# Kernel tuning notes

Hardware: AMD Instinct MI355X
Metric: run time of the kernel (lower is better)

Reference implementation:

```python
import jax, jax.numpy as jnp
import numpy as np

N_NODES = 50000
N_EDGES = 800000
HIDDEN = 128
N_LAYERS = 3
N_MASKED = 25000
N_GRAPHS = 64


def setup_inputs() -> dict:
    key = jax.random.key(0)
    ks = jax.random.split(key, 8)
    scale = 1.0 / np.sqrt(HIDDEN)
    return {
        "x": jax.random.normal(ks[0], (N_NODES, HIDDEN), dtype=jnp.float32),
        "edge_index": jax.random.randint(ks[1], (2, N_EDGES), 0, N_NODES, dtype=jnp.int64),
        "mask": jax.random.randint(ks[2], (N_MASKED,), 0, N_NODES, dtype=jnp.int64),
        "batch": jnp.sort(jax.random.randint(ks[3], (N_MASKED,), 0, N_GRAPHS, dtype=jnp.int64)),
        "conv_w": jax.random.normal(ks[4], (N_LAYERS, HIDDEN, HIDDEN), dtype=jnp.float32) * scale,
        "conv_b": jnp.zeros((N_LAYERS, HIDDEN), dtype=jnp.float32),
        "lt1_w": jax.random.normal(ks[5], (HIDDEN,), dtype=jnp.float32) * scale,
        "lt1_b": jnp.zeros((1,), dtype=jnp.float32),
    }


def reference(x, edge_index, mask, batch, conv_w, conv_b, lt1_w, lt1_b):
    n = x.shape[0]
    # GCNConv: add self-loops, symmetric normalization D^-1/2 (A+I) D^-1/2
    loops = jnp.arange(n, dtype=edge_index.dtype)
    src = jnp.concatenate([edge_index[0], loops])
    dst = jnp.concatenate([edge_index[1], loops])
    deg = jax.ops.segment_sum(jnp.ones_like(src, dtype=x.dtype), dst, num_segments=n)
    dinv = jax.lax.rsqrt(deg)  # deg >= 1 because of self-loops
    norm = (dinv[src] * dinv[dst])[:, None]  # [E+N, 1]

    h = x
    for l in range(N_LAYERS):
        hw = h @ conv_w[l]                                  # [N, H]
        agg = jax.ops.segment_sum(hw[src] * norm, dst, num_segments=n)
        h = jax.nn.elu(agg + conv_b[l])                     # dropout is identity in eval mode

    xm = h[mask]                                            # [M, H] masked-node features
    pooled = jax.ops.segment_max(xm, batch, num_segments=N_GRAPHS)  # global_max_pool
    return pooled @ lt1_w[:, None] + lt1_b                  # [G, 1]
```

## Files before the change

### kernel.cpp

```cpp
#include <hip/hip_runtime.h>
#include <math.h>

#define N_NODES  50000
#define N_EDGES  800000
#define HIDDEN   128
#define N_LAYERS 3
#define N_MASKED 25000
#define N_GRAPHS 64

typedef __attribute__((ext_vector_type(8))) short bf16x8;
typedef __attribute__((ext_vector_type(4))) float f32x4;

__device__ __forceinline__ unsigned fmap(float f) {
    unsigned u = __float_as_uint(f);
    return (u & 0x80000000u) ? ~u : (u | 0x80000000u);
}
__device__ __forceinline__ float funmap(unsigned u) {
    return __uint_as_float((u & 0x80000000u) ? (u & 0x7FFFFFFFu) : ~u);
}

__device__ __forceinline__ unsigned pack_split(float x) {
    unsigned u = __float_as_uint(x);
    unsigned hi = (u + 0x7fffu + ((u >> 16) & 1u)) >> 16;
    float rem = x - __uint_as_float(hi << 16);
    unsigned v = __float_as_uint(rem);
    unsigned lo = (v + 0x7fffu + ((v >> 16) & 1u)) >> 16;
    return hi | (lo << 16);
}

__global__ void count_deg_kernel(const int* __restrict__ dst, unsigned* __restrict__ deg) {
    int i = blockIdx.x * blockDim.x + threadIdx.x;
    if (i < N_EDGES) atomicAdd(&deg[dst[i]], 1u);
}

__global__ void dinv_kernel(const unsigned* __restrict__ deg, float* __restrict__ dinv) {
    int i = blockIdx.x * blockDim.x + threadIdx.x;
    if (i < N_NODES) dinv[i] = rsqrtf((float)(deg[i] + 1u));
}

__global__ void scan_block_kernel(const unsigned* __restrict__ deg, unsigned* __restrict__ incl,
                                  unsigned* __restrict__ bsum) {
    __shared__ unsigned s[1024];
    int i = blockIdx.x * 1024 + threadIdx.x;
    unsigned v = (i < N_NODES) ? deg[i] : 0u;
    s[threadIdx.x] = v;
    __syncthreads();
    for (int off = 1; off < 1024; off <<= 1) {
        unsigned t = (threadIdx.x >= off) ? s[threadIdx.x - off] : 0u;
        __syncthreads();
        s[threadIdx.x] += t;
        __syncthreads();
    }
    if (i < N_NODES) incl[i] = s[threadIdx.x];
    if (threadIdx.x == 1023) bsum[blockIdx.x] = s[1023];
}

__global__ void scan_bsum_kernel(unsigned* __restrict__ bsum, int n) {
    if (blockIdx.x == 0 && threadIdx.x == 0) {
        unsigned run = 0;
        for (int i = 0; i < n; ++i) { unsigned t = bsum[i]; bsum[i] = run; run += t; }
    }
}

__global__ void scan_finalize_kernel(const unsigned* __restrict__ incl,
                                     const unsigned* __restrict__ bsum_ex,
                                     unsigned* __restrict__ row_ptr,
                                     unsigned* __restrict__ cursor) {
    int i = blockIdx.x * blockDim.x + threadIdx.x;
    if (i <= N_NODES) {
        unsigned v = (i == 0) ? 0u : incl[i - 1] + bsum_ex[(i - 1) >> 10];
        row_ptr[i] = v;
        if (i < N_NODES) cursor[i] = v;
    }
}

__global__ void fill_csr_kernel(const int* __restrict__ src, const int* __restrict__ dst,
                                unsigned* __restrict__ cursor, int* __restrict__ csr_src) {
    int e = blockIdx.x * blockDim.x + threadIdx.x;
    if (e < N_EDGES) {
        unsigned p = atomicAdd(&cursor[dst[e]], 1u);
        csr_src[p] = src[e];
    }
}

__global__ void wprep_kernel(const float* __restrict__ W,
                             unsigned short* __restrict__ Whi,
                             unsigned short* __restrict__ Wlo) {
    int idx = blockIdx.x * 256 + threadIdx.x;
    if (idx >= 3 * 16384) return;
    int j     = idx & 7;
    int lane  = (idx >> 3) & 63;
    int ct    = (idx >> 9) & 7;
    int ks    = (idx >> 12) & 3;
    int layer = idx >> 14;
    int k = ks * 32 + (lane >> 4) * 8 + j;
    int n = ct * 16 + (lane & 15);
    unsigned p = pack_split(W[layer * 16384 + k * 128 + n]);
    Whi[idx] = (unsigned short)(p & 0xffffu);
    Wlo[idx] = (unsigned short)(p >> 16);
}

__global__ void xpack_kernel(const float* __restrict__ x, unsigned* __restrict__ xp, int n) {
    int i = blockIdx.x * 256 + threadIdx.x;
    if (i < n) xp[i] = pack_split(x[i]);
}

template<int MODE>
__global__ __launch_bounds__(256) void mfma_gemm_kernel(const unsigned* __restrict__ Ap,
                                                        const unsigned short* __restrict__ Wh,
                                                        const unsigned short* __restrict__ Wl,
                                                        const float* __restrict__ dinv,
                                                        const float* __restrict__ bias,
                                                        const int* __restrict__ batch,
                                                        unsigned* __restrict__ gmax,
                                                        float* __restrict__ Out,
                                                        int nrows) {
    const int lane = threadIdx.x & 63;
    const int wv = threadIdx.x >> 6;
    const int rowBase = blockIdx.x * 64 + wv * 16;
    if (rowBase >= nrows) return;

    int arow = rowBase + (lane & 15);
    if (arow > nrows - 1) arow = nrows - 1;
    const unsigned* aptr = Ap + (size_t)arow * 128 + (lane >> 4) * 8;

    f32x4 acc[8];
    #pragma unroll
    for (int c = 0; c < 8; ++c) acc[c] = (f32x4){0.f, 0.f, 0.f, 0.f};

    #pragma unroll
    for (int ks = 0; ks < 4; ++ks) {
        uint4 pa0 = *(const uint4*)(aptr + ks * 32);
        uint4 pa1 = *(const uint4*)(aptr + ks * 32 + 4);
        unsigned pv[8] = {pa0.x, pa0.y, pa0.z, pa0.w, pa1.x, pa1.y, pa1.z, pa1.w};
        bf16x8 ah, al;
        #pragma unroll
        for (int j = 0; j < 8; ++j) {
            ah[j] = (short)(pv[j] & 0xffffu);
            al[j] = (short)(pv[j] >> 16);
        }
        const unsigned short* wbh = Wh + ks * 4096 + lane * 8;
        const unsigned short* wbl = Wl + ks * 4096 + lane * 8;
        #pragma unroll
        for (int ct = 0; ct < 8; ++ct) {
            bf16x8 bh = *(const bf16x8*)(wbh + ct * 512);
            bf16x8 bl = *(const bf16x8*)(wbl + ct * 512);
            acc[ct] = __builtin_amdgcn_mfma_f32_16x16x32_bf16(ah, bh, acc[ct], 0, 0, 0);
            acc[ct] = __builtin_amdgcn_mfma_f32_16x16x32_bf16(al, bh, acc[ct], 0, 0, 0);
            acc[ct] = __builtin_amdgcn_mfma_f32_16x16x32_bf16(ah, bl, acc[ct], 0, 0, 0);
        }
    }

    const int colBase = lane & 15;
    const int rgrp = lane >> 4;
    #pragma unroll
    for (int r = 0; r < 4; ++r) {
        int row = rowBase + rgrp * 4 + r;
        if (row >= nrows) continue;
        float d = 0.f;
        int bofs = 0;
        if (MODE == 0 || MODE == 1) d = dinv[row];
        if (MODE == 2) bofs = batch[row] * 128;
        #pragma unroll
        for (int ct = 0; ct < 8; ++ct) {
            int col = ct * 16 + colBase;
            float o = acc[ct][r];
            if (MODE == 0) {
                Out[(size_t)row * 128 + col] = o * d;
            } else {
                o += bias[col];
                o = o > 0.f ? o : expm1f(o);
                if (MODE == 1) Out[(size_t)row * 128 + col] = o * d;
                else           atomicMax(&gmax[bofs + col], fmap(o));
            }
        }
    }
}

template<int GMODE>
__global__ __launch_bounds__(256) void gather_kernel(const float* __restrict__ tab,
                                                     const unsigned* __restrict__ row_ptr,
                                                     const int* __restrict__ csr_src,
                                                     const float* __restrict__ dinv,
                                                     const float* __restrict__ bias,
                                                     float* __restrict__ outf,
                                                     unsigned* __restrict__ outp,
                                                     const int* __restrict__ nodes,
                                                     int n_items) {
    int wid = (blockIdx.x * blockDim.x + threadIdx.x) >> 6;
    int w = wid >> 1;
    if (w >= n_items) return;
    const int f = ((wid & 1) << 6) | (threadIdx.x & 63);
    const int v = nodes ? nodes[w] : w;

    const unsigned s0 = row_ptr[v], e0 = row_ptr[v + 1];
    const float* __restrict__ base = tab + f;

    float acc[8];
    #pragma unroll
    for (int j = 0; j < 8; ++j) acc[j] = 0.f;
    acc[0] = base[(size_t)v << 7];

    unsigned i = s0;
    if (i + 8 <= e0) {
        int idx[8];
        #pragma unroll
        for (int j = 0; j < 8; ++j) idx[j] = csr_src[i + j];
        for (; i + 16 <= e0; i += 8) {
            int nxt[8];
            #pragma unroll
            for (int j = 0; j < 8; ++j) nxt[j] = csr_src[i + 8 + j];
            #pragma unroll
            for (int j = 0; j < 8; ++j) acc[j] += base[(size_t)idx[j] << 7];
            #pragma unroll
            for (int j = 0; j < 8; ++j) idx[j] = nxt[j];
        }
        #pragma unroll
        for (int j = 0; j < 8; ++j) acc[j] += base[(size_t)idx[j] << 7];
        i += 8;
    }
    if (i + 4 <= e0) {
        #pragma unroll
        for (int j = 0; j < 4; ++j) acc[j] += base[(size_t)csr_src[i + j] << 7];
        i += 4;
    }
    for (; i < e0; ++i) acc[0] += base[(size_t)csr_src[i] << 7];

    float dv = dinv[v];
    float sumall = ((acc[0] + acc[1]) + (acc[2] + acc[3])) +
                   ((acc[4] + acc[5]) + (acc[6] + acc[7]));
    if (GMODE == 0) {
        float o = dv * sumall + bias[f];
        o = o > 0.f ? o : expm1f(o);
        outf[((size_t)w << 7) + f] = o * dv;
    } else {
        outp[((size_t)w << 7) + f] = pack_split(dv * sumall);
    }
}

__global__ void gmax_init_kernel(unsigned* __restrict__ gmax) {
    int i = blockIdx.x * blockDim.x + threadIdx.x;
    if (i < N_GRAPHS * 128) gmax[i] = 0x007FFFFFu;
}

__global__ void pool_finish_kernel(const unsigned* __restrict__ gmax,
                                   const float* __restrict__ w, const float* __restrict__ b,
                                   float* __restrict__ out) {
    const int g = blockIdx.x;
    const int f = threadIdx.x;
    float val = funmap(gmax[g * 128 + f]) * w[f];
    #pragma unroll
    for (int off = 32; off > 0; off >>= 1) val += __shfl_down(val, off);
    __shared__ float ps[2];
    if ((threadIdx.x & 63) == 0) ps[threadIdx.x >> 6] = val;
    __syncthreads();
    if (threadIdx.x == 0) out[g] = ps[0] + ps[1] + b[0];
}

extern "C" void kernel_launch(void* const* d_in, const int* in_sizes, int n_in,
                              void* d_out, int out_size, void* d_ws, size_t ws_size,
                              hipStream_t stream) {
    const float* x      = (const float*)d_in[0];
    const int*   ei     = (const int*)d_in[1];
    const int*   mask   = (const int*)d_in[2];
    const int*   batch  = (const int*)d_in[3];
    const float* conv_w = (const float*)d_in[4];
    const float* conv_b = (const float*)d_in[5];
    const float* lt1_w  = (const float*)d_in[6];
    const float* lt1_b  = (const float*)d_in[7];
    float* out = (float*)d_out;

    const int* e_src = ei;
    const int* e_dst = ei + N_EDGES;

    char* ws = (char*)d_ws;
    auto carve = [&](size_t bytes) { char* p = ws; ws += (bytes + 255) & ~(size_t)255; return p; };
    unsigned* deg     = (unsigned*)carve(N_NODES * 4);
    float*    dinv    = (float*)   carve(N_NODES * 4);
    unsigned* row_ptr = (unsigned*)carve((N_NODES + 1) * 4);
    unsigned* cursor  = (unsigned*)carve(N_NODES * 4);
    unsigned* bsum    = (unsigned*)carve(64 * 4);
    unsigned* gmax    = (unsigned*)carve(N_GRAPHS * 128 * 4);
    unsigned short* wph = (unsigned short*)carve(3 * 16384 * 2);
    unsigned short* wpl = (unsigned short*)carve(3 * 16384 * 2);
    int*      csr_src = (int*)     carve((size_t)N_EDGES * 4);
    char*     reg1    = carve((size_t)N_NODES * HIDDEN * 4);
    char*     reg2    = carve((size_t)N_NODES * HIDDEN * 4);
    unsigned* incl    = (unsigned*)csr_src;

    unsigned* xp    = (unsigned*)reg1;
    float*    bufB  = (float*)reg1;
    float*    bufB2 = (float*)reg1;
    float*    bufA  = (float*)reg2;
    unsigned* bufAp = (unsigned*)reg2;
    unsigned* bufCp = (unsigned*)reg2;

    const int NB_SCAN = (N_NODES + 1023) / 1024;

    hipMemsetAsync(deg, 0, N_NODES * sizeof(unsigned), stream);
    count_deg_kernel<<<(N_EDGES + 255) / 256, 256, 0, stream>>>(e_dst, deg);
    dinv_kernel<<<(N_NODES + 255) / 256, 256, 0, stream>>>(deg, dinv);
    scan_block_kernel<<<NB_SCAN, 1024, 0, stream>>>(deg, incl, bsum);
    scan_bsum_kernel<<<1, 64, 0, stream>>>(bsum, NB_SCAN);
    scan_finalize_kernel<<<(N_NODES + 256) / 256, 256, 0, stream>>>(incl, bsum, row_ptr, cursor);
    fill_csr_kernel<<<(N_EDGES + 255) / 256, 256, 0, stream>>>(e_src, e_dst, cursor, csr_src);
    gmax_init_kernel<<<(N_GRAPHS * 128 + 255) / 256, 256, 0, stream>>>(gmax);
    wprep_kernel<<<(3 * 16384 + 255) / 256, 256, 0, stream>>>(conv_w, wph, wpl);
    xpack_kernel<<<(N_NODES * HIDDEN + 255) / 256, 256, 0, stream>>>(x, xp, N_NODES * HIDDEN);

    const int GEMM_FULL = (N_NODES + 63) / 64;
    const int GEMM_MASK = (N_MASKED + 63) / 64;
    const int GA_FULL = (N_NODES * 2 * 64 + 255) / 256;
    const int GA_MASK = (N_MASKED * 2 * 64 + 255) / 256;

    mfma_gemm_kernel<0><<<GEMM_FULL, 256, 0, stream>>>(xp, wph, wpl, dinv, nullptr,
                                                       nullptr, nullptr, bufA, N_NODES);
    gather_kernel<0><<<GA_FULL, 256, 0, stream>>>(bufA, row_ptr, csr_src, dinv,
                                                  conv_b, bufB, nullptr, nullptr, N_NODES);
    gather_kernel<1><<<GA_FULL, 256, 0, stream>>>(bufB, row_ptr, csr_src, dinv,
                                                  nullptr, nullptr, bufAp, nullptr, N_NODES);
    mfma_gemm_kernel<1><<<GEMM_FULL, 256, 0, stream>>>(bufAp, wph + 16384, wpl + 16384, dinv,
                                                       conv_b + HIDDEN, nullptr, nullptr,
                                                       bufB2, N_NODES);
    gather_kernel<1><<<GA_MASK, 256, 0, stream>>>(bufB2, row_ptr, csr_src, dinv,
                                                  nullptr, nullptr, bufCp, mask, N_MASKED);
    mfma_gemm_kernel<2><<<GEMM_MASK, 256, 0, stream>>>(bufCp, wph + 32768, wpl + 32768, nullptr,
                                                       conv_b + 2 * HIDDEN, batch, gmax,
                                                       nullptr, N_MASKED);

    pool_finish_kernel<<<N_GRAPHS, HIDDEN, 0, stream>>>(gmax, lt1_w, lt1_b, out);
}
```

Measured before the change: 394.7 us.

## Stage GEMM A tiles and split weights into LDS via direct global-to-LDS loads

The MFMA GEMM now uses 512-thread blocks covering 128 rows. Each block copies its packed A tile (64KB) and the hi/lo bf16 weight halves (64KB) into 128KB of LDS using global_load_lds before computing. Operands are then read from LDS instead of each wave reading weights straight from global memory or cache. This adds a large LDS footprint and a block-wide barrier, which may limit occupancy and removes any overlap between loading and compute.

```diff
diff --git a/kernel.cpp b/kernel.cpp
--- a/kernel.cpp
+++ b/kernel.cpp
@@ -10,6 +10,10 @@
 
 typedef __attribute__((ext_vector_type(8))) short bf16x8;
 typedef __attribute__((ext_vector_type(4))) float f32x4;
+
+#define GLOAD_LDS16(g, l) \
+    __builtin_amdgcn_global_load_lds((const __attribute__((address_space(1))) void*)(g), \
+                                     (__attribute__((address_space(3))) void*)(l), 16, 0, 0)
 
 __device__ __forceinline__ unsigned fmap(float f) {
     unsigned u = __float_as_uint(f);
@@ -106,23 +110,43 @@
 }
 
 template<int MODE>
-__global__ __launch_bounds__(256) void mfma_gemm_kernel(const unsigned* __restrict__ Ap,
-                                                        const unsigned short* __restrict__ Wh,
-                                                        const unsigned short* __restrict__ Wl,
-                                                        const float* __restrict__ dinv,
-                                                        const float* __restrict__ bias,
-                                                        const int* __restrict__ batch,
-                                                        unsigned* __restrict__ gmax,
-                                                        float* __restrict__ Out,
-                                                        int nrows) {
-    const int lane = threadIdx.x & 63;
-    const int wv = threadIdx.x >> 6;
-    const int rowBase = blockIdx.x * 64 + wv * 16;
-    if (rowBase >= nrows) return;
-
-    int arow = rowBase + (lane & 15);
-    if (arow > nrows - 1) arow = nrows - 1;
-    const unsigned* aptr = Ap + (size_t)arow * 128 + (lane >> 4) * 8;
+__global__ __launch_bounds__(512, 2) void mfma_gemm_kernel(const unsigned* __restrict__ Ap,
+                                                           const unsigned short* __restrict__ Wh,
+                                                           const unsigned short* __restrict__ Wl,
+                                                           const float* __restrict__ dinv,
+                                                           const float* __restrict__ bias,
+                                                           const int* __restrict__ batch,
+                                                           unsigned* __restrict__ gmax,
+                                                           float* __restrict__ Out,
+                                                           int nrows) {
+    extern __shared__ char smem[];
+    const int tid = threadIdx.x;
+    const int lane = tid & 63;
+    const int w = tid >> 6;
+    const int blockRow = blockIdx.x * 128;
+
+    #pragma unroll
+    for (int i = 0; i < 8; ++i) {
+        int n0 = w * 512 + i * 64;
+        int n = n0 + lane;
+        int L  = n & 63;
+        int h  = (n >> 6) & 1;
+        int ks = (n >> 7) & 3;
+        int wb = (n >> 9) & 7;
+        int row = blockRow + wb * 16 + (L & 15);
+        if (row > nrows - 1) row = nrows - 1;
+        const unsigned* g = Ap + (size_t)row * 128 + ks * 32 + ((L >> 4) * 8) + h * 4;
+        GLOAD_LDS16(g, smem + (size_t)n0 * 16);
+    }
+    #pragma unroll
+    for (int i = 0; i < 4; ++i) {
+        int m0 = w * 256 + i * 64;
+        GLOAD_LDS16((const char*)Wh + (size_t)(m0 + lane) * 16, smem + 65536 + (size_t)m0 * 16);
+        GLOAD_LDS16((const char*)Wl + (size_t)(m0 + lane) * 16, smem + 98304 + (size_t)m0 * 16);
+    }
+    __syncthreads();
+
+    if (blockRow + w * 16 >= nrows) return;
 
     f32x4 acc[8];
     #pragma unroll
@@ -130,21 +154,21 @@
 
     #pragma unroll
     for (int ks = 0; ks < 4; ++ks) {
-        uint4 pa0 = *(const uint4*)(aptr + ks * 32);
-        uint4 pa1 = *(const uint4*)(aptr + ks * 32 + 4);
-        unsigned pv[8] = {pa0.x, pa0.y, pa0.z, pa0.w, pa1.x, pa1.y, pa1.z, pa1.w};
+        uint4 a0 = *(const uint4*)(smem + (size_t)(((w * 4 + ks) * 2 + 0) * 1024) + lane * 16);
+        uint4 a1 = *(const uint4*)(smem + (size_t)(((w * 4 + ks) * 2 + 1) * 1024) + lane * 16);
+        unsigned pv[8] = {a0.x, a0.y, a0.z, a0.w, a1.x, a1.y, a1.z, a1.w};
         bf16x8 ah, al;
         #pragma unroll
         for (int j = 0; j < 8; ++j) {
             ah[j] = (short)(pv[j] & 0xffffu);
             al[j] = (short)(pv[j] >> 16);
         }
-        const unsigned short* wbh = Wh + ks * 4096 + lane * 8;
-        const unsigned short* wbl = Wl + ks * 4096 + lane * 8;
+        const char* wbh = smem + 65536 + ks * 8192 + lane * 16;
+        const char* wbl = smem + 98304 + ks * 8192 + lane * 16;
         #pragma unroll
         for (int ct = 0; ct < 8; ++ct) {
-            bf16x8 bh = *(const bf16x8*)(wbh + ct * 512);
-            bf16x8 bl = *(const bf16x8*)(wbl + ct * 512);
+            bf16x8 bh = *(const bf16x8*)(wbh + ct * 1024);
+            bf16x8 bl = *(const bf16x8*)(wbl + ct * 1024);
             acc[ct] = __builtin_amdgcn_mfma_f32_16x16x32_bf16(ah, bh, acc[ct], 0, 0, 0);
             acc[ct] = __builtin_amdgcn_mfma_f32_16x16x32_bf16(al, bh, acc[ct], 0, 0, 0);
             acc[ct] = __builtin_amdgcn_mfma_f32_16x16x32_bf16(ah, bl, acc[ct], 0, 0, 0);
@@ -155,7 +179,7 @@
     const int rgrp = lane >> 4;
     #pragma unroll
     for (int r = 0; r < 4; ++r) {
-        int row = rowBase + rgrp * 4 + r;
+        int row = blockRow + w * 16 + rgrp * 4 + r;
         if (row >= nrows) continue;
         float d = 0.f;
         int bofs = 0;
@@ -308,25 +332,26 @@
     wprep_kernel<<<(3 * 16384 + 255) / 256, 256, 0, stream>>>(conv_w, wph, wpl);
     xpack_kernel<<<(N_NODES * HIDDEN + 255) / 256, 256, 0, stream>>>(x, xp, N_NODES * HIDDEN);
 
-    const int GEMM_FULL = (N_NODES + 63) / 64;
-    const int GEMM_MASK = (N_MASKED + 63) / 64;
+    const int GEMM_FULL = (N_NODES + 127) / 128;
+    const int GEMM_MASK = (N_MASKED + 127) / 128;
     const int GA_FULL = (N_NODES * 2 * 64 + 255) / 256;
     const int GA_MASK = (N_MASKED * 2 * 64 + 255) / 256;
-
-    mfma_gemm_kernel<0><<<GEMM_FULL, 256, 0, stream>>>(xp, wph, wpl, dinv, nullptr,
-                                                       nullptr, nullptr, bufA, N_NODES);
+    const size_t LDS_BYTES = 131072;
+
+    mfma_gemm_kernel<0><<<GEMM_FULL, 512, LDS_BYTES, stream>>>(xp, wph, wpl, dinv, nullptr,
+                                                               nullptr, nullptr, bufA, N_NODES);
     gather_kernel<0><<<GA_FULL, 256, 0, stream>>>(bufA, row_ptr, csr_src, dinv,
                                                   conv_b, bufB, nullptr, nullptr, N_NODES);
     gather_kernel<1><<<GA_FULL, 256, 0, stream>>>(bufB, row_ptr, csr_src, dinv,
                                                   nullptr, nullptr, bufAp, nullptr, N_NODES);
-    mfma_gemm_kernel<1><<<GEMM_FULL, 256, 0, stream>>>(bufAp, wph + 16384, wpl + 16384, dinv,
-                                                       conv_b + HIDDEN, nullptr, nullptr,
-                                                       bufB2, N_NODES);
+    mfma_gemm_kernel<1><<<GEMM_FULL, 512, LDS_BYTES, stream>>>(bufAp, wph + 16384, wpl + 16384,
+                                                               dinv, conv_b + HIDDEN, nullptr,
+                                                               nullptr, bufB2, N_NODES);
     gather_kernel<1><<<GA_MASK, 256, 0, stream>>>(bufB2, row_ptr, csr_src, dinv,
                                                   nullptr, nullptr, bufCp, mask, N_MASKED);
-    mfma_gemm_kernel<2><<<GEMM_MASK, 256, 0, stream>>>(bufCp, wph + 32768, wpl + 32768, nullptr,
-                                                       conv_b + 2 * HIDDEN, batch, gmax,
-                                                       nullptr, N_MASKED);
+    mfma_gemm_kernel<2><<<GEMM_MASK, 512, LDS_BYTES, stream>>>(bufCp, wph + 32768, wpl + 32768,
+                                                               nullptr, conv_b + 2 * HIDDEN,
+                                                               batch, gmax, nullptr, N_MASKED);
 
     pool_finish_kernel<<<N_GRAPHS, HIDDEN, 0, stream>>>(gmax, lt1_w, lt1_b, out);
 }
```

New measurement: 393.9 us. No clear change (-0.2%).
